# Optimization experiments

Hardware: AMD Instinct MI355X
Metric: run time of the kernel (lower is better)

The kernel has to match this reference:

```python
import jax, jax.numpy as jnp
import numpy as np

N_NODES, N_EDGES, F_DIM, H_DIM = 50000, 800000, 128, 128
BN_EPS = 1e-3  # keras BatchNormalization default epsilon


def setup_inputs() -> dict:
    key = jax.random.key(0)
    k0, k1, k2 = jax.random.split(key, 3)
    edge_pairs = jax.random.randint(k0, (N_EDGES, 2), 0, N_NODES, dtype=jnp.int64 if jax.config.jax_enable_x64 else jnp.int32)
    node_features = jax.random.normal(k1, (N_NODES, F_DIM), dtype=jnp.float32)
    W = jax.random.normal(k2, (F_DIM, H_DIM), dtype=jnp.float32) * (1.0 / np.sqrt(F_DIM))
    b = jnp.zeros((H_DIM,), jnp.float32)
    gamma = jnp.ones((H_DIM,), jnp.float32)
    beta = jnp.zeros((H_DIM,), jnp.float32)
    moving_mean = jnp.zeros((H_DIM,), jnp.float32)
    moving_var = jnp.ones((H_DIM,), jnp.float32)
    return {"edge_pairs": edge_pairs, "node_features": node_features, "W": W, "b": b,
            "gamma": gamma, "beta": beta, "moving_mean": moving_mean, "moving_var": moving_var}


def reference(edge_pairs, node_features, W, b, gamma, beta, moving_mean, moving_var):
    src = edge_pairs[:, 0]
    dst = edge_pairs[:, 1]
    n = node_features.shape[0]

    # linear transform (dropout inactive: training=False)
    t = node_features @ W + b  # [N, H]

    # out-degree by source node
    deg = jax.ops.segment_sum(jnp.ones(src.shape[0], t.dtype), src, num_segments=n)  # [N]
    inv_sqrt_deg = jnp.power(deg, -0.5)  # matches tf.pow(d, -0.5)

    # degree-normalized neighbour messages: d_src^-1/2 * d_dst^-1/2 * t[dst]
    scale = (inv_sqrt_deg[src] * inv_sqrt_deg[dst])[:, None]  # [E,1]
    nb_sum = jax.ops.segment_sum(t[dst] * scale, src, num_segments=n)  # [N, H]

    # source term: segment_mean(deg[src] * t[src]) ; empty segments -> 0 (tf semantics)
    msg = deg[src][:, None] * t[src]  # [E, H]
    seg = jax.ops.segment_sum(msg, src, num_segments=n)  # [N, H]
    src_mean = jnp.where(deg[:, None] > 0, seg / jnp.maximum(deg, 1.0)[:, None], 0.0)

    agg = 0.5 * nb_sum + 0.5 * src_mean

    # batchnorm, inference mode (moving statistics)
    return (agg - moving_mean) * jax.lax.rsqrt(moving_var + BN_EPS) * gamma + beta
```

## Files before the change

### kernel.cpp

```cpp
#include <hip/hip_runtime.h>
#include <math.h>

#define BN_EPS 0.001f
#define CHUNK 2048
#define MAXBUCK 1024

typedef __attribute__((ext_vector_type(8))) short bf16x8;
typedef __attribute__((ext_vector_type(4))) float f32x4;
typedef __attribute__((ext_vector_type(2))) float f32x2;

__device__ inline unsigned bf16rne(float f) {
  unsigned u = __float_as_uint(f);
  return (u + 0x7fffu + ((u >> 16) & 1u)) >> 16;
}

__global__ __launch_bounds__(256) void k_ehist(const int2* __restrict__ ep, int ne,
                                               int nbuck, int* __restrict__ ghist) {
  __shared__ int h[MAXBUCK];
  int c = blockIdx.x, t = threadIdx.x;
  for (int i = t; i < nbuck; i += 256) h[i] = 0;
  __syncthreads();
  int base = c * CHUNK;
  int end = min(base + CHUNK, ne);
  for (int e = base + t; e < end; e += 256) atomicAdd(&h[ep[e].x >> 6], 1);
  __syncthreads();
  int* row = ghist + (size_t)c * nbuck;
  for (int i = t; i < nbuck; i += 256) row[i] = h[i];
}

__global__ __launch_bounds__(512) void k_bscan(int* __restrict__ ghist, int nchunk,
                                               int nbuck, int* __restrict__ btot) {
  __shared__ int s0[512], s1[512];
  int b = blockIdx.x, t = threadIdx.x;
  int v = (t < nchunk) ? ghist[(size_t)t * nbuck + b] : 0;
  s0[t] = v;
  __syncthreads();
  int* src = s0; int* dst = s1;
  for (int off = 1; off < 512; off <<= 1) {
    int x = src[t];
    if (t >= off) x += src[t - off];
    dst[t] = x;
    __syncthreads();
    int* tmp = src; src = dst; dst = tmp;
  }
  if (t < nchunk) ghist[(size_t)t * nbuck + b] = src[t] - v;
  if (t == 0) btot[b] = src[511];
}

__global__ __launch_bounds__(1024) void k_bbase(const int* __restrict__ btot, int nbuck,
                                                int* __restrict__ bbase) {
  __shared__ int s0[1024], s1[1024];
  int t = threadIdx.x;
  int v = (t < nbuck) ? btot[t] : 0;
  s0[t] = v;
  __syncthreads();
  int* src = s0; int* dst = s1;
  for (int off = 1; off < 1024; off <<= 1) {
    int x = src[t];
    if (t >= off) x += src[t - off];
    dst[t] = x;
    __syncthreads();
    int* tmp = src; src = dst; dst = tmp;
  }
  if (t < nbuck) bbase[t] = src[t] - v;
}

__global__ __launch_bounds__(256) void k_ebin(const int2* __restrict__ ep, int ne,
                                              int nbuck, const int* __restrict__ ghist,
                                              const int* __restrict__ bbase,
                                              unsigned* __restrict__ bins) {
  __shared__ int cur[MAXBUCK];
  int c = blockIdx.x, t = threadIdx.x;
  const int* row = ghist + (size_t)c * nbuck;
  for (int i = t; i < nbuck; i += 256) cur[i] = bbase[i] + row[i];
  __syncthreads();
  int base = c * CHUNK;
  int end = min(base + CHUNK, ne);
  for (int e = base + t; e < end; e += 256) {
    int2 p = ep[e];
    int pos = atomicAdd(&cur[p.x >> 6], 1);
    bins[pos] = (unsigned)p.y | ((unsigned)(p.x & 63) << 17);
  }
}

__global__ __launch_bounds__(256) void k_bfinal(const int* __restrict__ bbase,
                                                const int* __restrict__ btot,
                                                const unsigned* __restrict__ bins,
                                                int n, int* __restrict__ deg,
                                                float* __restrict__ isd,
                                                int* __restrict__ offsets,
                                                int* __restrict__ csr_dst) {
  __shared__ int h[64];
  __shared__ int cur[64];
  int bk = blockIdx.x, t = threadIdx.x;
  if (t < 64) h[t] = 0;
  __syncthreads();
  int s = bbase[bk], cnt = btot[bk];
  for (int i = t; i < cnt; i += 256) atomicAdd(&h[bins[s + i] >> 17], 1);
  __syncthreads();
  if (t == 0) {
    int run = s;
    for (int j = 0; j < 64; ++j) { cur[j] = run; run += h[j]; }
  }
  __syncthreads();
  if (t < 64) {
    int node = (bk << 6) + t;
    if (node < n) {
      deg[node] = h[t];
      offsets[node] = cur[t];
      isd[node] = 1.0f / sqrtf((float)h[t]);
    }
  }
  __syncthreads();
  for (int i = t; i < cnt; i += 256) {
    unsigned r = bins[s + i];
    int pos = atomicAdd(&cur[r >> 17], 1);
    csr_dst[pos] = (int)(r & 0x1FFFFu);
  }
}

__global__ __launch_bounds__(1024, 4) void k_gemm(const float* __restrict__ X,
                                                  const float* __restrict__ W,
                                                  const float* __restrict__ b,
                                                  const float* __restrict__ isd,
                                                  float* __restrict__ T,
                                                  unsigned char* __restrict__ Tb8, int M) {
  __shared__ unsigned short WhL[16384];
  __shared__ unsigned short WlL[16384];
  int tid = threadIdx.x;

#pragma unroll
  for (int it = 0; it < 4; ++it) {
    int q = tid + it * 1024;
    int k = q >> 5;
    int c0 = (q & 31) * 4;
    float4 v = ((const float4*)W)[q];
    float vv[4] = {v.x, v.y, v.z, v.w};
#pragma unroll
    for (int j2 = 0; j2 < 4; ++j2) {
      int col = c0 + j2;
      float x = vv[j2];
      unsigned short hh = (unsigned short)(__float_as_uint(x) >> 16);
      float rem = x - __uint_as_float((unsigned)hh << 16);
      int frag = ((col >> 4) << 2) | (k >> 5);
      int ln = (((k >> 3) & 3) << 4) | (col & 15);
      int addr = frag * 512 + ln * 8 + (k & 7);
      WhL[addr] = hh;
      WlL[addr] = (unsigned short)bf16rne(rem);
    }
  }

  int wave = tid >> 6, lane = tid & 63;
  int r16 = lane & 15, kq = lane >> 4;
  int rowbase = blockIdx.x * 256 + wave * 16;
  int arow = rowbase + r16;
  bool aok = arow < M;
  const float* xr = X + ((size_t)arow << 7);

  bf16x8 ah[4], al[4];
#pragma unroll
  for (int ks = 0; ks < 4; ++ks) {
    int k0 = ks * 32 + kq * 8;
    float4 v0 = aok ? *(const float4*)(xr + k0) : make_float4(0.f, 0.f, 0.f, 0.f);
    float4 v1 = aok ? *(const float4*)(xr + k0 + 4) : make_float4(0.f, 0.f, 0.f, 0.f);
    float f[8] = {v0.x, v0.y, v0.z, v0.w, v1.x, v1.y, v1.z, v1.w};
    bf16x8 h8, l8;
#pragma unroll
    for (int j = 0; j < 8; ++j) {
      unsigned short hh = (unsigned short)(__float_as_uint(f[j]) >> 16);
      float rem = f[j] - __uint_as_float((unsigned)hh << 16);
      h8[j] = (short)hh;
      l8[j] = (short)bf16rne(rem);
    }
    ah[ks] = h8;
    al[ks] = l8;
  }
  __syncthreads();

  f32x4 acc[8] = {};
#pragma unroll
  for (int ct = 0; ct < 8; ++ct) {
#pragma unroll
    for (int ks = 0; ks < 4; ++ks) {
      int base = (ct * 4 + ks) * 512 + lane * 8;
      bf16x8 bh = *(const bf16x8*)&WhL[base];
      bf16x8 bl = *(const bf16x8*)&WlL[base];
      acc[ct] = __builtin_amdgcn_mfma_f32_16x16x32_bf16(ah[ks], bh, acc[ct], 0, 0, 0);
      acc[ct] = __builtin_amdgcn_mfma_f32_16x16x32_bf16(ah[ks], bl, acc[ct], 0, 0, 0);
      acc[ct] = __builtin_amdgcn_mfma_f32_16x16x32_bf16(al[ks], bh, acc[ct], 0, 0, 0);
    }
  }

  int orow[4];
  float isdr[4];
#pragma unroll
  for (int r = 0; r < 4; ++r) {
    orow[r] = rowbase + kq * 4 + r;
    isdr[r] = (orow[r] < M) ? isd[orow[r]] : 0.f;
  }
#pragma unroll
  for (int ct = 0; ct < 8; ++ct) {
    int col = ct * 16 + r16;
    float bias = b[col];
#pragma unroll
    for (int r = 0; r < 4; ++r) {
      float v = acc[ct][r] + bias;
      bool ok = orow[r] < M;
      if (ok) T[((size_t)orow[r] << 7) + col] = v;
      float sv = v * isdr[r];
      float other = __shfl_xor(sv, 1);
      int pk01 = __builtin_amdgcn_cvt_pk_fp8_f32(sv, other, 0, false);
      int pk23 = __shfl_xor(pk01, 2);
      if (ok && (r16 & 3) == 0) {
        unsigned dword = ((unsigned)pk01 & 0xFFFFu) | ((unsigned)pk23 << 16);
        *(unsigned*)&Tb8[((size_t)orow[r] << 7) + ct * 16 + r16] = dword;
      }
    }
  }
}

__global__ __launch_bounds__(256) void k_gather(
    const float* __restrict__ T, const unsigned char* __restrict__ Tb8,
    const int* __restrict__ deg, const float* __restrict__ isd,
    const int* __restrict__ offsets, const int* __restrict__ csr_dst,
    const float* __restrict__ mm, const float* __restrict__ var,
    const float* __restrict__ gamma, const float* __restrict__ beta,
    float* __restrict__ out, int n, int ne) {
  int wave = threadIdx.x >> 6;
  int lane = threadIdx.x & 63;
  int i = blockIdx.x * 4 + wave;
  if (i >= n) return;
  int degi = deg[i];
  int start = offsets[i];
  const unsigned short* rows = (const unsigned short*)Tb8;
  float sx[16] = {}, sy[16] = {};
  for (int e = 0; e < degi; e += 16) {
    int ii = start + e + (lane & 15);
    int dv = (ii < ne) ? csr_dst[ii] : 0;
    unsigned short r[16];
#pragma unroll
    for (int j = 0; j < 16; ++j) {
      int idx = __shfl(dv, j);
      r[j] = rows[((size_t)idx << 6) + lane];
    }
#pragma unroll
    for (int j = 0; j < 16; ++j) {
      int rr = (e + j < degi) ? (int)r[j] : 0;
      f32x2 f = __builtin_amdgcn_cvt_pk_f32_fp8(rr, false);
      sx[j] += f.x;
      sy[j] += f.y;
    }
  }
  float fx = (((sx[0] + sx[1]) + (sx[2] + sx[3])) + ((sx[4] + sx[5]) + (sx[6] + sx[7]))) +
             (((sx[8] + sx[9]) + (sx[10] + sx[11])) + ((sx[12] + sx[13]) + (sx[14] + sx[15])));
  float fy = (((sy[0] + sy[1]) + (sy[2] + sy[3])) + ((sy[4] + sy[5]) + (sy[6] + sy[7]))) +
             (((sy[8] + sy[9]) + (sy[10] + sy[11])) + ((sy[12] + sy[13]) + (sy[14] + sy[15])));
  float aggx = 0.f, aggy = 0.f;
  if (degi > 0) {
    float2 tv = ((const float2*)(T + ((size_t)i << 7)))[lane];
    float isi = isd[i];
    float di = (float)degi;
    aggx = 0.5f * (isi * fx) + 0.5f * (di * tv.x);
    aggy = 0.5f * (isi * fy) + 0.5f * (di * tv.y);
  }
  float2 mmv = ((const float2*)mm)[lane];
  float2 vv = ((const float2*)var)[lane];
  float2 gv = ((const float2*)gamma)[lane];
  float2 bv = ((const float2*)beta)[lane];
  float2 res;
  res.x = (aggx - mmv.x) * rsqrtf(vv.x + BN_EPS) * gv.x + bv.x;
  res.y = (aggy - mmv.y) * rsqrtf(vv.y + BN_EPS) * gv.y + bv.y;
  ((float2*)(out + ((size_t)i << 7)))[lane] = res;
}

static inline size_t align_up(size_t x) { return (x + 255) & ~(size_t)255; }

extern "C" void kernel_launch(void* const* d_in, const int* in_sizes, int n_in,
                              void* d_out, int out_size, void* d_ws, size_t ws_size,
                              hipStream_t stream) {
  const int2* ep = (const int2*)d_in[0];
  const float* X = (const float*)d_in[1];
  const float* W = (const float*)d_in[2];
  const float* b = (const float*)d_in[3];
  const float* gamma = (const float*)d_in[4];
  const float* beta = (const float*)d_in[5];
  const float* mm = (const float*)d_in[6];
  const float* var = (const float*)d_in[7];
  float* out = (float*)d_out;

  const int ne = in_sizes[0] / 2;
  const int n = in_sizes[1] / 128;
  const int nbuck = (n + 63) >> 6;
  const int nchunk = (ne + CHUNK - 1) / CHUNK;

  char* p = (char*)d_ws;
  int* deg = (int*)p;        p += align_up((size_t)n * 4);
  float* isd = (float*)p;    p += align_up((size_t)n * 4);
  int* offsets = (int*)p;    p += align_up((size_t)n * 4);
  int* btot = (int*)p;       p += align_up((size_t)nbuck * 4);
  int* bbase = (int*)p;      p += align_up((size_t)nbuck * 4);
  int* ghist = (int*)p;      p += align_up((size_t)nchunk * nbuck * 4);
  int* csr_dst = (int*)p;    p += align_up((size_t)ne * 4);
  unsigned* bins = (unsigned*)p; p += align_up((size_t)ne * 4);
  float* T = (float*)p;      p += align_up((size_t)n * 128 * 4);
  unsigned char* Tb8 = (unsigned char*)p; p += align_up((size_t)n * 128);

  k_ehist<<<nchunk, 256, 0, stream>>>(ep, ne, nbuck, ghist);
  k_bscan<<<nbuck, 512, 0, stream>>>(ghist, nchunk, nbuck, btot);
  k_bbase<<<1, 1024, 0, stream>>>(btot, nbuck, bbase);
  k_ebin<<<nchunk, 256, 0, stream>>>(ep, ne, nbuck, ghist, bbase, bins);
  k_bfinal<<<nbuck, 256, 0, stream>>>(bbase, btot, bins, n, deg, isd, offsets, csr_dst);
  k_gemm<<<(n + 255) / 256, 1024, 0, stream>>>(X, W, b, isd, T, Tb8, n);
  k_gather<<<(n + 3) / 4, 256, 0, stream>>>(T, Tb8, deg, isd, offsets, csr_dst,
                                            mm, var, gamma, beta, out, n, ne);
}
```

Baseline: 92.49 us.

## Process two nodes per wave in gather with 4-byte fp8 row loads

The gather kernel now assigns two destination nodes to each 64-lane wave, one per 32-lane half. Each lane loads four fp8 values (a dword) per neighbour instead of two, and the neighbour batch drops from 16 to 8. This halves the wave count and widens each memory access, cutting per-node overhead and load instruction count. The cost is divergence when the two nodes' degrees differ, since the loop runs to the larger of the two degrees.

```diff
diff --git a/kernel.cpp b/kernel.cpp
--- a/kernel.cpp
+++ b/kernel.cpp
@@ -225,52 +225,65 @@
     const int* __restrict__ offsets, const int* __restrict__ csr_dst,
     const float* __restrict__ mm, const float* __restrict__ var,
     const float* __restrict__ gamma, const float* __restrict__ beta,
-    float* __restrict__ out, int n, int ne) {
+    float* __restrict__ out, int n) {
   int wave = threadIdx.x >> 6;
   int lane = threadIdx.x & 63;
-  int i = blockIdx.x * 4 + wave;
-  if (i >= n) return;
-  int degi = deg[i];
-  int start = offsets[i];
-  const unsigned short* rows = (const unsigned short*)Tb8;
-  float sx[16] = {}, sy[16] = {};
-  for (int e = 0; e < degi; e += 16) {
-    int ii = start + e + (lane & 15);
-    int dv = (ii < ne) ? csr_dst[ii] : 0;
-    unsigned short r[16];
-#pragma unroll
-    for (int j = 0; j < 16; ++j) {
-      int idx = __shfl(dv, j);
-      r[j] = rows[((size_t)idx << 6) + lane];
-    }
-#pragma unroll
-    for (int j = 0; j < 16; ++j) {
-      int rr = (e + j < degi) ? (int)r[j] : 0;
-      f32x2 f = __builtin_amdgcn_cvt_pk_f32_fp8(rr, false);
-      sx[j] += f.x;
-      sy[j] += f.y;
-    }
-  }
-  float fx = (((sx[0] + sx[1]) + (sx[2] + sx[3])) + ((sx[4] + sx[5]) + (sx[6] + sx[7]))) +
-             (((sx[8] + sx[9]) + (sx[10] + sx[11])) + ((sx[12] + sx[13]) + (sx[14] + sx[15])));
-  float fy = (((sy[0] + sy[1]) + (sy[2] + sy[3])) + ((sy[4] + sy[5]) + (sy[6] + sy[7]))) +
-             (((sy[8] + sy[9]) + (sy[10] + sy[11])) + ((sy[12] + sy[13]) + (sy[14] + sy[15])));
-  float aggx = 0.f, aggy = 0.f;
+  int half = lane >> 5;
+  int l32 = lane & 31;
+  int pair = blockIdx.x * 4 + wave;
+  int i = 2 * pair + half;
+  if (2 * pair >= n) return;
+  bool iok = i < n;
+  int degi = iok ? deg[i] : 0;
+  int start = iok ? offsets[i] : 0;
+  int dother = __shfl(degi, lane ^ 32);
+  int dmax = max(degi, dother);
+  const unsigned* rows = (const unsigned*)Tb8;
+
+  f32x4 acc[8] = {};
+  for (int e = 0; e < dmax; e += 8) {
+    int sl = l32 & 7;
+    int dv = (e + sl < degi) ? csr_dst[start + e + sl] : i;
+    unsigned r8[8];
+#pragma unroll
+    for (int j = 0; j < 8; ++j) {
+      int idx = __shfl(dv, (half << 5) + j);
+      r8[j] = rows[((size_t)idx << 5) + l32];
+    }
+#pragma unroll
+    for (int j = 0; j < 8; ++j) {
+      int rr = (e + j < degi) ? (int)r8[j] : 0;
+      f32x2 f01 = __builtin_amdgcn_cvt_pk_f32_fp8(rr, false);
+      f32x2 f23 = __builtin_amdgcn_cvt_pk_f32_fp8(rr, true);
+      acc[j][0] += f01.x;
+      acc[j][1] += f01.y;
+      acc[j][2] += f23.x;
+      acc[j][3] += f23.y;
+    }
+  }
+  f32x4 s = ((acc[0] + acc[1]) + (acc[2] + acc[3])) + ((acc[4] + acc[5]) + (acc[6] + acc[7]));
+
+  if (!iok) return;
+  float4 aggv = make_float4(0.f, 0.f, 0.f, 0.f);
   if (degi > 0) {
-    float2 tv = ((const float2*)(T + ((size_t)i << 7)))[lane];
+    float4 tv = ((const float4*)(T + ((size_t)i << 7)))[l32];
     float isi = isd[i];
     float di = (float)degi;
-    aggx = 0.5f * (isi * fx) + 0.5f * (di * tv.x);
-    aggy = 0.5f * (isi * fy) + 0.5f * (di * tv.y);
-  }
-  float2 mmv = ((const float2*)mm)[lane];
-  float2 vv = ((const float2*)var)[lane];
-  float2 gv = ((const float2*)gamma)[lane];
-  float2 bv = ((const float2*)beta)[lane];
-  float2 res;
-  res.x = (aggx - mmv.x) * rsqrtf(vv.x + BN_EPS) * gv.x + bv.x;
-  res.y = (aggy - mmv.y) * rsqrtf(vv.y + BN_EPS) * gv.y + bv.y;
-  ((float2*)(out + ((size_t)i << 7)))[lane] = res;
+    aggv.x = 0.5f * (isi * s[0]) + 0.5f * (di * tv.x);
+    aggv.y = 0.5f * (isi * s[1]) + 0.5f * (di * tv.y);
+    aggv.z = 0.5f * (isi * s[2]) + 0.5f * (di * tv.z);
+    aggv.w = 0.5f * (isi * s[3]) + 0.5f * (di * tv.w);
+  }
+  float4 mmv = ((const float4*)mm)[l32];
+  float4 vv = ((const float4*)var)[l32];
+  float4 gv = ((const float4*)gamma)[l32];
+  float4 bv = ((const float4*)beta)[l32];
+  float4 res;
+  res.x = (aggv.x - mmv.x) * rsqrtf(vv.x + BN_EPS) * gv.x + bv.x;
+  res.y = (aggv.y - mmv.y) * rsqrtf(vv.y + BN_EPS) * gv.y + bv.y;
+  res.z = (aggv.z - mmv.z) * rsqrtf(vv.z + BN_EPS) * gv.z + bv.z;
+  res.w = (aggv.w - mmv.w) * rsqrtf(vv.w + BN_EPS) * gv.w + bv.w;
+  ((float4*)(out + ((size_t)i << 7)))[l32] = res;
 }
 
 static inline size_t align_up(size_t x) { return (x + 255) & ~(size_t)255; }
@@ -311,6 +324,7 @@
   k_ebin<<<nchunk, 256, 0, stream>>>(ep, ne, nbuck, ghist, bbase, bins);
   k_bfinal<<<nbuck, 256, 0, stream>>>(bbase, btot, bins, n, deg, isd, offsets, csr_dst);
   k_gemm<<<(n + 255) / 256, 1024, 0, stream>>>(X, W, b, isd, T, Tb8, n);
-  k_gather<<<(n + 3) / 4, 256, 0, stream>>>(T, Tb8, deg, isd, offsets, csr_dst,
-                                            mm, var, gamma, beta, out, n, ne);
-}
+  int pairs = (n + 1) / 2;
+  k_gather<<<(pairs + 3) / 4, 256, 0, stream>>>(T, Tb8, deg, isd, offsets, csr_dst,
+                                                mm, var, gamma, beta, out, n);
+}
```

Result: faster. 81.82 us (-11.5%).
